# Performance work log

Hardware: AMD Instinct MI355X
Metric: run time of the kernel (lower is better)

Reference implementation:

```python
import jax, jax.numpy as jnp
import numpy as np

B, S, DIM = 2, 2048, 2048
NH, NKV = 16, 4
HD = DIM // NH
BASE, FACTOR = 10000.0, 1.0
WINDOW, STRIDE = 256, 64


def setup_inputs() -> dict:
    key = jax.random.key(0)
    ks = jax.random.split(key, 5)
    x = jax.random.normal(ks[0], (B, S, DIM), jnp.float32)
    Wq = jax.random.normal(ks[1], (DIM, DIM), jnp.float32) * 0.02
    Wkv = jax.random.normal(ks[2], (2 * NKV * HD, DIM), jnp.float32) * 0.02
    Wo = jax.random.normal(ks[3], (DIM, DIM), jnp.float32) * 0.02
    Wr = jax.random.normal(ks[4], (NH, DIM), jnp.float32) * 0.02
    br = jnp.zeros((NH,), jnp.float32)
    return {"x": x, "Wq": Wq, "Wkv": Wkv, "Wo": Wo, "Wr": Wr, "br": br}


def _rope_cos_sin(seqlen, start_pos):
    half = HD // 2
    inv_freq = 1.0 / (BASE ** (jnp.arange(0, half, dtype=jnp.float32) * 2.0 / HD))
    inv_freq = inv_freq / FACTOR  # YaRN position interpolation; FACTOR=1 -> vanilla RoPE
    mscale = float(0.1 * np.log(FACTOR) + 1.0) if FACTOR > 1.0 else 1.0
    t = jnp.arange(start_pos, start_pos + seqlen, dtype=jnp.float32)
    freqs = t[:, None] * inv_freq[None, :]  # [S, HD/2]
    return jnp.cos(freqs) * mscale, jnp.sin(freqs) * mscale


def _apply_rope(x, cos, sin):
    # x: [B, H, S, HD]; rotate-half convention
    x1, x2 = jnp.split(x, 2, axis=-1)
    return jnp.concatenate([x1 * cos - x2 * sin, x2 * cos + x1 * sin], axis=-1)


def reference(x, Wq, Wkv, Wo, Wr, br):
    scale = 1.0 / np.sqrt(HD)
    # projections
    q = (x @ Wq.T).reshape(B, S, NH, HD).transpose(0, 2, 1, 3)        # [B,NH,S,HD]
    kv = (x @ Wkv.T).reshape(B, S, 2, NKV, HD)
    k = kv[:, :, 0].transpose(0, 2, 1, 3)                              # [B,NKV,S,HD]
    v = kv[:, :, 1].transpose(0, 2, 1, 3)
    # RoPE (start_pos = 0)
    cos, sin = _rope_cos_sin(S, 0)
    cos, sin = cos[None, None], sin[None, None]
    q = _apply_rope(q, cos, sin)
    k = _apply_rope(k, cos, sin)
    # GQA expansion (repeat_interleave over head axis)
    rep = NH // NKV
    k = jnp.repeat(k, rep, axis=1)                                     # [B,NH,S,HD]
    v = jnp.repeat(v, rep, axis=1)
    # per-head sigmoid routing gate on q
    head_w = jax.nn.sigmoid(x @ Wr.T + br)                             # [B,S,NH]
    q = q * head_w.transpose(0, 2, 1)[..., None]
    # local windowed causal attention
    qi = jnp.arange(S)[:, None]
    ki = jnp.arange(S)[None, :]
    mask = (ki <= qi) & (ki >= qi - WINDOW)                            # [S,S]
    scores = jnp.einsum('bhqd,bhkd->bhqk', q, k) * scale
    scores = jnp.where(mask, scores, -1e30)
    attn_local = jnp.einsum('bhqk,bhkd->bhqd', jax.nn.softmax(scores, axis=-1), v)
    # strided global attention (non-causal over subsampled keys)
    g_idx = jnp.arange(0, S, STRIDE)
    kg, vg = k[:, :, g_idx], v[:, :, g_idx]                            # [B,NH,S/STRIDE,HD]
    gscores = jnp.einsum('bhqd,bhkd->bhqk', q, kg) * scale
    attn_global = jnp.einsum('bhqk,bhkd->bhqd', jax.nn.softmax(gscores, axis=-1), vg)
    out = 0.7 * attn_local + 0.3 * attn_global
    out = out.transpose(0, 2, 1, 3).reshape(B, S, DIM)
    return out @ Wo.T
```

## Files before the change

### kernel.cpp

```cpp
#include <hip/hip_runtime.h>
#include <stdint.h>

typedef unsigned short u16;
typedef uint32_t u32;
typedef __bf16 bf16x8 __attribute__((ext_vector_type(8)));
typedef u16    u16x8  __attribute__((ext_vector_type(8)));
typedef float  f32x4  __attribute__((ext_vector_type(4)));
typedef u32    u32x4v __attribute__((ext_vector_type(4)));

constexpr int Bc = 2, Sc = 2048, DIMc = 2048, NHc = 16, NKVc = 4, HDc = 128;
constexpr int Mc  = Bc * Sc;
constexpr int QKVN = 3072;
constexpr float SCALE = 0.08838834764831845f;

__device__ __forceinline__ u16 f2bf(float f) {
    uint32_t u = __builtin_bit_cast(uint32_t, f);
    u += 0x7FFFu + ((u >> 16) & 1u);
    return (u16)(u >> 16);
}
__device__ __forceinline__ u32 pk2bf(float a, float b) {
    return (u32)f2bf(a) | ((u32)f2bf(b) << 16);
}

__device__ __forceinline__ void async_cp16(const u16* gsrc, u16* ldst) {
    __builtin_amdgcn_global_load_lds(
        (__attribute__((address_space(1))) void*)(gsrc),
        (__attribute__((address_space(3))) void*)(ldst), 16, 0, 0);
}

constexpr int HWB = Mc;
constexpr int CQ1 = DIMc * DIMc / 4;
constexpr int CQ2 = 1024 * DIMc / 4;
constexpr int NWQ = (CQ1 + CQ2) / 256;
constexpr int NTB = Sc * 64 / 256;
__global__ __launch_bounds__(256) void cvt_hw(const float* __restrict__ x,
                                              const float* __restrict__ Wq,
                                              const float* __restrict__ Wkv,
                                              const float* __restrict__ Wr,
                                              const float* __restrict__ br,
                                              u16* __restrict__ xb,
                                              u16* __restrict__ Wqkvb,
                                              float* __restrict__ hw,
                                              float2* __restrict__ csT) {
    __shared__ __align__(16) float xs[2048];
    int bid = blockIdx.x;
    if (bid < HWB) {
        const int m = bid;
        const float4* xg = (const float4*)(x + (size_t)m * 2048);
        float4* xs4 = (float4*)xs;
        for (int i = threadIdx.x; i < 512; i += 256) xs4[i] = xg[i];
        __syncthreads();
        {
            ushort4* dst = (ushort4*)(xb + (size_t)m * 2048);
            for (int i = threadIdx.x; i < 512; i += 256) {
                float4 v = xs4[i];
                ushort4 o;
                o.x = f2bf(v.x); o.y = f2bf(v.y); o.z = f2bf(v.z); o.w = f2bf(v.w);
                dst[i] = o;
            }
        }
        const int wid = threadIdx.x >> 6, lane = threadIdx.x & 63;
#pragma unroll 1
        for (int h = wid; h < NHc; h += 4) {
            const float4* wr4 = (const float4*)(Wr + (size_t)h * 2048);
            float s = 0.f;
#pragma unroll
            for (int j = 0; j < 8; j++) {
                float4 xv = xs4[lane + j * 64];
                float4 wv = wr4[lane + j * 64];
                s += xv.x * wv.x + xv.y * wv.y + xv.z * wv.z + xv.w * wv.w;
            }
#pragma unroll
            for (int off = 32; off; off >>= 1) s += __shfl_xor(s, off, 64);
            if (lane == 0) hw[m * NHc + h] = 1.f / (1.f + __expf(-(s + br[h])));
        }
        return;
    }
    bid -= HWB;
    if (bid < NWQ) {
        int q = bid * 256 + threadIdx.x;
        const float* src; u16* dst; int qi;
        if (q < CQ1) { src = Wq;  dst = Wqkvb; qi = q; }
        else         { src = Wkv; dst = Wqkvb + (size_t)DIMc * DIMc; qi = q - CQ1; }
        float4 v = ((const float4*)src)[qi];
        ushort4 o;
        o.x = f2bf(v.x); o.y = f2bf(v.y); o.z = f2bf(v.z); o.w = f2bf(v.w);
        ((ushort4*)dst)[qi] = o;
        return;
    }
    bid -= NWQ;
    int idx = bid * 256 + threadIdx.x;
    int s = idx >> 6, d = idx & 63;
    float invf = powf(10000.0f, -(float)d * (1.0f / 64.0f));
    float ang = (float)s * invf;
    float2 cs;
    cs.x = cosf(ang);
    cs.y = sinf(ang);
    csT[idx] = cs;
}

__global__ __launch_bounds__(512, 2) void gemm_qkv(const u16* __restrict__ A,
                                                   const u16* __restrict__ Bw,
                                                   const float* __restrict__ hw,
                                                   const float2* __restrict__ csT,
                                                   const float* __restrict__ Wo,
                                                   u16* __restrict__ Wob,
                                                   u16* __restrict__ Qr,
                                                   u16* __restrict__ Kb,
                                                   u16* __restrict__ Vt,
                                                   u16* __restrict__ Vg) {
    const int bidL = blockIdx.x;
    if (bidL >= 192) {
        const float4* src = (const float4*)Wo;
        ushort4* dst = (ushort4*)Wob;
        int i0 = (bidL - 192) * 16384 + threadIdx.x;
#pragma unroll
        for (int k = 0; k < 32; k++) {
            float4 v = src[i0 + k * 512];
            ushort4 o;
            o.x = f2bf(v.x); o.y = f2bf(v.y); o.z = f2bf(v.z); o.w = f2bf(v.w);
            dst[i0 + k * 512] = o;
        }
        return;
    }
    __shared__ __align__(16) u16 SM[4][2][128 * 64];
    float* EpS = (float*)SM;
    const int Kd = DIMc;
    constexpr int NT = 32;
    const int tid  = threadIdx.x;
    const int lane = tid & 63;
    const int wid  = tid >> 6;
    const int m0 = (bidL / 12) * 256;
    const int n0 = (bidL % 12) * 256;
    const int wr = wid >> 2;
    const int wc = wid & 3;
    const int fr = lane & 15;
    const int fq = lane >> 4;
    const int f7 = fr & 7;

    const int s0 = tid, s1 = tid + 512;
    const int r0 = s0 >> 3, r1 = s1 >> 3;
    const int j0 = (s0 & 7) ^ (r0 & 7), j1 = (s1 & 7) ^ (r1 & 7);
    const u16* gA0 = A  + (size_t)(m0 + r0) * Kd + j0 * 8;
    const u16* gA1 = A  + (size_t)(m0 + r1) * Kd + j1 * 8;
    const u16* gB0 = Bw + (size_t)(n0 + r0) * Kd + j0 * 8;
    const u16* gB1 = Bw + (size_t)(n0 + r1) * Kd + j1 * 8;
    const size_t hK = (size_t)128 * Kd;

    auto stA = [&](int buf, int h, int t) {
        async_cp16(gA0 + h * hK + t * 64, &SM[buf][h][s0 * 8]);
        async_cp16(gA1 + h * hK + t * 64, &SM[buf][h][s1 * 8]);
    };
    auto stB = [&](int buf, int h, int t) {
        async_cp16(gB0 + h * hK + t * 64, &SM[2 + buf][h][s0 * 8]);
        async_cp16(gB1 + h * hK + t * 64, &SM[2 + buf][h][s1 * 8]);
    };

    f32x4 acc[8][4];
#pragma unroll
    for (int i = 0; i < 8; i++)
#pragma unroll
        for (int j = 0; j < 4; j++) {
            f32x4 z = {0.f, 0.f, 0.f, 0.f};
            acc[i][j] = z;
        }

    const int c0 = ((fq) ^ f7) * 8;
    const int c1 = ((4 + fq) ^ f7) * 8;
    bf16x8 afl[4][2], afh[4][2], bfl[2][2], bfh[2][2];

    auto rdA = [&](bf16x8 (&af)[4][2], int tb, int mh) {
        const u16* Ab = SM[tb][wr];
#pragma unroll
        for (int m2 = 0; m2 < 4; m2++) {
            int row = (mh * 4 + m2) * 16 + fr;
            af[m2][0] = __builtin_bit_cast(bf16x8, *(const u16x8*)(Ab + row * 64 + c0));
            af[m2][1] = __builtin_bit_cast(bf16x8, *(const u16x8*)(Ab + row * 64 + c1));
        }
    };
    auto rdB = [&](bf16x8 (&bf)[2][2], int tb, int nh) {
        const u16* Bb = SM[2 + tb][wc >> 1];
#pragma unroll
        for (int n2 = 0; n2 < 2; n2++) {
            int row = (wc & 1) * 64 + (nh * 2 + n2) * 16 + fr;
            bf[n2][0] = __builtin_bit_cast(bf16x8, *(const u16x8*)(Bb + row * 64 + c0));
            bf[n2][1] = __builtin_bit_cast(bf16x8, *(const u16x8*)(Bb + row * 64 + c1));
        }
    };
    auto mma = [&](bf16x8 (&af)[4][2], bf16x8 (&bf)[2][2], int mh, int nh) {
        __builtin_amdgcn_s_setprio(1);
#pragma unroll
        for (int m2 = 0; m2 < 4; m2++)
#pragma unroll
            for (int n2 = 0; n2 < 2; n2++) {
                acc[mh * 4 + m2][nh * 2 + n2] =
                    __builtin_amdgcn_mfma_f32_16x16x32_bf16(af[m2][0], bf[n2][0],
                                                            acc[mh * 4 + m2][nh * 2 + n2], 0, 0, 0);
                acc[mh * 4 + m2][nh * 2 + n2] =
                    __builtin_amdgcn_mfma_f32_16x16x32_bf16(af[m2][1], bf[n2][1],
                                                            acc[mh * 4 + m2][nh * 2 + n2], 0, 0, 0);
            }
        __builtin_amdgcn_s_setprio(0);
    };

#define LGK0 do { asm volatile("s_waitcnt lgkmcnt(0)" ::: "memory"); \
                  __builtin_amdgcn_sched_barrier(0); } while (0)
#define BAR  __builtin_amdgcn_s_barrier()

    stA(0, 0, 0); stA(0, 1, 0); stB(0, 0, 0); stB(0, 1, 0);
    stB(1, 0, 1); stB(1, 1, 1);
    asm volatile("s_waitcnt vmcnt(4)" ::: "memory");
    BAR;

#pragma unroll 1
    for (int i = 0; i < NT / 2; i++) {
        const int t0 = 2 * i, t1 = 2 * i + 1;
        rdA(afl, 0, 0); rdB(bfl, 0, 0);
        stA(1, 0, t1);
        BAR; LGK0; mma(afl, bfl, 0, 0); BAR;
        rdB(bfh, 0, 1);
        stA(1, 1, t1);
        BAR; LGK0; mma(afl, bfh, 0, 1); BAR;
        rdA(afh, 0, 1);
        if (t0 + 2 < NT) stB(0, 0, t0 + 2);
        BAR; LGK0; mma(afh, bfl, 1, 0); BAR;
        if (t0 + 2 < NT) {
            stB(0, 1, t0 + 2);
            asm volatile("s_waitcnt vmcnt(4)" ::: "memory");
        } else {
            asm volatile("s_waitcnt vmcnt(0)" ::: "memory");
        }
        BAR; __builtin_amdgcn_sched_barrier(0); mma(afh, bfh, 1, 1); BAR;
        rdA(afl, 1, 0); rdB(bfl, 1, 0);
        if (t0 + 2 < NT) stA(0, 0, t0 + 2);
        BAR; LGK0; mma(afl, bfl, 0, 0); BAR;
        rdB(bfh, 1, 1);
        if (t0 + 2 < NT) stA(0, 1, t0 + 2);
        BAR; LGK0; mma(afl, bfh, 0, 1); BAR;
        rdA(afh, 1, 1);
        if (t1 + 2 < NT) stB(1, 0, t1 + 2);
        BAR; LGK0; mma(afh, bfl, 1, 0); BAR;
        if (t1 + 2 < NT) {
            stB(1, 1, t1 + 2);
            asm volatile("s_waitcnt vmcnt(4)" ::: "memory");
        } else {
            asm volatile("s_waitcnt vmcnt(0)" ::: "memory");
        }
        BAR; __builtin_amdgcn_sched_barrier(0); mma(afh, bfh, 1, 1); BAR;
    }
#undef LGK0
#undef BAR

    const int tL = n0 >> 7;
    const int bb = m0 >> 11;
    const int sb_t = m0 & 2047;
#pragma unroll
    for (int p = 0; p < 4; p++) {
        __syncthreads();
        if (wr == (p >> 1)) {
#pragma unroll
            for (int m2 = 0; m2 < 4; m2++) {
#pragma unroll
                for (int nj = 0; nj < 4; nj++) {
                    int lr = m2 * 16 + fq * 4;
                    int col = wc * 64 + nj * 16 + fr;
#pragma unroll
                    for (int r = 0; r < 4; r++)
                        EpS[(lr + r) * 261 + col] = acc[(p & 1) * 4 + m2][nj][r];
                }
            }
        }
        __syncthreads();
        const int sbase = sb_t + p * 64;
        if (tL < 20) {
            const int d = tid & 63, rg = tid >> 6;
#pragma unroll 1
            for (int ch = 0; ch < 2; ch++) {
                const int t = tL + ch;
#pragma unroll
                for (int tt = 0; tt < 8; tt++) {
                    int lr = rg + 8 * tt;
                    int s = sbase + lr;
                    float v1 = EpS[lr * 261 + ch * 128 + d];
                    float v2 = EpS[lr * 261 + ch * 128 + 64 + d];
                    float2 cs = csT[(s << 6) + d];
                    float o1 = v1 * cs.x - v2 * cs.y;
                    float o2 = v2 * cs.x + v1 * cs.y;
                    if (t < 16) {
                        float w = hw[(size_t)((bb << 11) + s) * NHc + t] * SCALE;
                        size_t g = ((size_t)(bb * NHc + t) << 11) + s;
                        Qr[g * HDc + d]      = f2bf(o1 * w);
                        Qr[g * HDc + 64 + d] = f2bf(o2 * w);
                    } else {
                        size_t g = ((size_t)(bb * NKVc + (t - 16)) << 11) + s;
                        Kb[g * HDc + d]      = f2bf(o1);
                        Kb[g * HDc + 64 + d] = f2bf(o2);
                    }
                }
            }
        } else {
            const int sl = tid & 63, dg = tid >> 6;
            const int sg = sbase + sl;
#pragma unroll 1
            for (int ch = 0; ch < 2; ch++) {
                const int bhv = bb * NKVc + (tL + ch - 20);
                u16* Vbase = Vt + (size_t)bhv * HDc * Sc;
#pragma unroll
                for (int tt = 0; tt < 16; tt++) {
                    int d = dg + 8 * tt;
                    u16 bv = f2bf(EpS[sl * 261 + ch * 128 + d]);
                    Vbase[(size_t)d * Sc + sg] = bv;
                    if ((sg & 63) == 0)
                        Vg[(size_t)bhv * 4096 + d * 32 + (sg >> 6)] = bv;
                }
            }
        }
    }
}

__global__ __launch_bounds__(512, 2) void gemm_bt3(const u16* __restrict__ A,
                                                   const u16* __restrict__ Bw,
                                                   float* __restrict__ C,
                                                   int Mdim, int Ndim, int Kdim) {
    __shared__ __align__(16) u16 As[2][256 * 64];
    __shared__ __align__(16) u16 Bs[2][128 * 64];
    const int tid  = threadIdx.x;
    const int lane = tid & 63;
    const int wid  = tid >> 6;
    const int m0 = blockIdx.y * 256;
    const int n0 = blockIdx.x * 128;
    const int wm = (wid >> 1) * 64;
    const int wn = (wid & 1) * 64;
    const int fr = lane & 15;
    const int fq = lane >> 4;
    const int f7 = fr & 7;

    const u16* gA[4]; const u16* gB[2];
    int sOffA[4], sOffB[2];
#pragma unroll
    for (int q = 0; q < 4; q++) {
        int s = tid + q * 512;
        int row = s >> 3;
        int j = (s & 7) ^ (row & 7);
        gA[q] = A + (size_t)(m0 + row) * Kdim + j * 8;
        sOffA[q] = s * 8;
    }
#pragma unroll
    for (int q = 0; q < 2; q++) {
        int s = tid + q * 512;
        int row = s >> 3;
        int j = (s & 7) ^ (row & 7);
        gB[q] = Bw + (size_t)(n0 + row) * Kdim + j * 8;
        sOffB[q] = s * 8;
    }

    f32x4 acc[4][4];
#pragma unroll
    for (int i = 0; i < 4; i++)
#pragma unroll
        for (int j = 0; j < 4; j++) {
            f32x4 z = {0.f, 0.f, 0.f, 0.f};
            acc[i][j] = z;
        }

    const int NT = Kdim >> 6;
    const int c0 = ((fq) ^ f7) * 8;
    const int c1 = ((4 + fq) ^ f7) * 8;

#pragma unroll
    for (int q = 0; q < 4; q++) async_cp16(gA[q], &As[0][sOffA[q]]);
#pragma unroll
    for (int q = 0; q < 2; q++) async_cp16(gB[q], &Bs[0][sOffB[q]]);
#pragma unroll
    for (int q = 0; q < 4; q++) async_cp16(gA[q] + 64, &As[1][sOffA[q]]);
#pragma unroll
    for (int q = 0; q < 2; q++) async_cp16(gB[q] + 64, &Bs[1][sOffB[q]]);

    for (int t = 0; t < NT; t++) {
        const u16* At = As[t & 1];
        const u16* Bt = Bs[t & 1];

        if (t + 1 < NT) {
            asm volatile("s_waitcnt vmcnt(6)" ::: "memory");
        } else {
            asm volatile("s_waitcnt vmcnt(0)" ::: "memory");
        }
        __builtin_amdgcn_s_barrier();

        bf16x8 af0[4], bf0[4];
#pragma unroll
        for (int i = 0; i < 4; i++)
            af0[i] = __builtin_bit_cast(bf16x8, *(const u16x8*)(At + (wm + i * 16 + fr) * 64 + c0));
#pragma unroll
        for (int j = 0; j < 4; j++)
            bf0[j] = __builtin_bit_cast(bf16x8, *(const u16x8*)(Bt + (wn + j * 16 + fr) * 64 + c0));
        asm volatile("s_waitcnt lgkmcnt(0)" ::: "memory");
        __builtin_amdgcn_sched_barrier(0);
        __builtin_amdgcn_s_setprio(1);
#pragma unroll
        for (int i = 0; i < 2; i++)
#pragma unroll
            for (int j = 0; j < 4; j++)
                acc[i][j] = __builtin_amdgcn_mfma_f32_16x16x32_bf16(af0[i], bf0[j], acc[i][j], 0, 0, 0);
        __builtin_amdgcn_s_setprio(0);

        bf16x8 af1[4], bf1[4];
#pragma unroll
        for (int i = 0; i < 4; i++)
            af1[i] = __builtin_bit_cast(bf16x8, *(const u16x8*)(At + (wm + i * 16 + fr) * 64 + c1));
#pragma unroll
        for (int j = 0; j < 4; j++)
            bf1[j] = __builtin_bit_cast(bf16x8, *(const u16x8*)(Bt + (wn + j * 16 + fr) * 64 + c1));
        __builtin_amdgcn_s_setprio(1);
#pragma unroll
        for (int i = 2; i < 4; i++)
#pragma unroll
            for (int j = 0; j < 4; j++)
                acc[i][j] = __builtin_amdgcn_mfma_f32_16x16x32_bf16(af0[i], bf0[j], acc[i][j], 0, 0, 0);
        __builtin_amdgcn_s_setprio(0);
        asm volatile("s_waitcnt lgkmcnt(0)" ::: "memory");
        __builtin_amdgcn_sched_barrier(0);
        __builtin_amdgcn_s_barrier();

        if (t + 2 < NT) {
#pragma unroll
            for (int q = 0; q < 4; q++)
                async_cp16(gA[q] + (size_t)(t + 2) * 64, &As[t & 1][sOffA[q]]);
        }
        __builtin_amdgcn_s_setprio(1);
#pragma unroll
        for (int i = 0; i < 2; i++)
#pragma unroll
            for (int j = 0; j < 4; j++)
                acc[i][j] = __builtin_amdgcn_mfma_f32_16x16x32_bf16(af1[i], bf1[j], acc[i][j], 0, 0, 0);
        __builtin_amdgcn_s_setprio(0);

        if (t + 2 < NT) {
#pragma unroll
            for (int q = 0; q < 2; q++)
                async_cp16(gB[q] + (size_t)(t + 2) * 64, &Bs[t & 1][sOffB[q]]);
        }
        __builtin_amdgcn_s_setprio(1);
#pragma unroll
        for (int i = 2; i < 4; i++)
#pragma unroll
            for (int j = 0; j < 4; j++)
                acc[i][j] = __builtin_amdgcn_mfma_f32_16x16x32_bf16(af1[i], bf1[j], acc[i][j], 0, 0, 0);
        __builtin_amdgcn_s_setprio(0);
    }

#pragma unroll
    for (int i = 0; i < 4; i++)
#pragma unroll
        for (int j = 0; j < 4; j++) {
            int row = m0 + wm + i * 16 + fq * 4;
            int col = n0 + wn + j * 16 + fr;
#pragma unroll
            for (int r = 0; r < 4; r++)
                C[(size_t)(row + r) * Ndim + col] = acc[i][j][r];
        }
}

__device__ __forceinline__ float colreduce_max(f32x4 a, f32x4 b) {
    float m = fmaxf(fmaxf(fmaxf(a[0], a[1]), fmaxf(a[2], a[3])),
                    fmaxf(fmaxf(b[0], b[1]), fmaxf(b[2], b[3])));
    m = fmaxf(m, __shfl_xor(m, 16, 64));
    m = fmaxf(m, __shfl_xor(m, 32, 64));
    return m;
}

__device__ __forceinline__ bf16x8 build_pfrag(u32 pk0, u32 pk1, u32 pk2, u32 pk3, int lane) {
    const int c = lane & 15, Q = lane >> 4;
    const int sl0 = ((Q & 1) * 2) * 16 + c;
    const int sl1 = sl0 + 16;
    u32 a0 = (u32)__shfl((int)pk0, sl0, 64), b0 = (u32)__shfl((int)pk2, sl0, 64);
    u32 a1 = (u32)__shfl((int)pk1, sl0, 64), b1 = (u32)__shfl((int)pk3, sl0, 64);
    u32 a2 = (u32)__shfl((int)pk0, sl1, 64), b2 = (u32)__shfl((int)pk2, sl1, 64);
    u32 a3 = (u32)__shfl((int)pk1, sl1, 64), b3 = (u32)__shfl((int)pk3, sl1, 64);
    const bool hi = Q >= 2;
    u32x4v r = { hi ? b0 : a0, hi ? b1 : a1, hi ? b2 : a2, hi ? b3 : a3 };
    return __builtin_bit_cast(bf16x8, r);
}

__global__ __launch_bounds__(256) void attn3(const u16* __restrict__ Qr,
                                             const u16* __restrict__ Kb,
                                             const u16* __restrict__ Vt,
                                             const u16* __restrict__ Vg,
                                             u16* __restrict__ attnb) {
    __shared__ __align__(16) u16 Ksh[2 * 4096];
    __shared__ __align__(16) u16 Vsh[2 * 4096];
    const int tid  = threadIdx.x;
    const int lane = tid & 63, wid = tid >> 6;
    const int bid  = blockIdx.x;
    const int q64  = (31 - (bid >> 5)) << 6;
    const int bh   = bid & 31;
    const int h    = bh & 15;
    const int b    = bh >> 4;
    const int qw   = q64 + wid * 16;
    const int c = lane & 15, Q = lane >> 4;
    const int kvh = h >> 2;

    const u16* Qp = Qr + ((size_t)((b * NHc + h) * Sc + qw)) * HDc;
    const u16* Kh = Kb + (size_t)(b * NKVc + kvh) * Sc * HDc;
    const u16* Vh = Vt + (size_t)(b * NKVc + kvh) * HDc * Sc;
    const u16* Vgh = Vg + (size_t)(b * NKVc + kvh) * HDc * 32;

    const int kp0 = (q64 >= 256) ? (q64 - 256) : 0;
    const int nstages = (q64 + 64 - kp0) >> 5;

    auto stageLoad = [&](int bufi, int kp) {
        u16* Kd = Ksh + bufi * 4096;
        u16* Vd = Vsh + bufi * 4096;
#pragma unroll
        for (int qq = 0; qq < 2; qq++) {
            int s = tid + qq * 256;
            int kr = s >> 4;
            int jk = (s & 15) ^ (kr & 15);
            async_cp16(Kh + (size_t)(kp + kr) * HDc + jk * 8, Kd + s * 8);
            int dv = s >> 2;
            int jv = (s & 3) ^ ((dv >> 2) & 3);
            async_cp16(Vh + (size_t)dv * Sc + kp + jv * 8, Vd + s * 8);
        }
    };

    bf16x8 qf[4];
#pragma unroll
    for (int ch = 0; ch < 4; ch++)
        qf[ch] = __builtin_bit_cast(bf16x8, *(const u16x8*)(Qp + c * HDc + ch * 32 + Q * 8));

    stageLoad(0, kp0);

    f32x4 sg0 = {0.f,0.f,0.f,0.f}, sg1 = {0.f,0.f,0.f,0.f};
#pragma unroll
    for (int ch = 0; ch < 4; ch++) {
        bf16x8 k0 = __builtin_bit_cast(bf16x8, *(const u16x8*)(Kh + ((size_t)c << 6) * HDc + ch * 32 + Q * 8));
        bf16x8 k1 = __builtin_bit_cast(bf16x8, *(const u16x8*)(Kh + ((size_t)(c + 16) << 6) * HDc + ch * 32 + Q * 8));
        sg0 = __builtin_amdgcn_mfma_f32_16x16x32_bf16(k0, qf[ch], sg0, 0, 0, 0);
        sg1 = __builtin_amdgcn_mfma_f32_16x16x32_bf16(k1, qf[ch], sg1, 0, 0, 0);
    }
    float mg = colreduce_max(sg0, sg1);
    f32x4 pg0, pg1;
    float gsum = 0.f;
#pragma unroll
    for (int r = 0; r < 4; r++) {
        pg0[r] = __expf(sg0[r] - mg);
        pg1[r] = __expf(sg1[r] - mg);
        gsum += pg0[r] + pg1[r];
    }
    gsum += __shfl_xor(gsum, 16, 64);
    gsum += __shfl_xor(gsum, 32, 64);
    const float lG = gsum;
    bf16x8 pgf = build_pfrag(pk2bf(pg0[0], pg0[1]), pk2bf(pg0[2], pg0[3]),
                             pk2bf(pg1[0], pg1[1]), pk2bf(pg1[2], pg1[3]), lane);
    f32x4 OG[8];
#pragma unroll
    for (int dt = 0; dt < 8; dt++) {
        bf16x8 vf = __builtin_bit_cast(bf16x8, *(const u16x8*)(Vgh + (dt * 16 + c) * 32 + Q * 8));
        f32x4 z = {0.f, 0.f, 0.f, 0.f};
        OG[dt] = __builtin_amdgcn_mfma_f32_16x16x32_bf16(vf, pgf, z, 0, 0, 0);
    }

    f32x4 OL[8];
#pragma unroll
    for (int dt = 0; dt < 8; dt++) { f32x4 z = {0.f,0.f,0.f,0.f}; OL[dt] = z; }
    float mL = -1e30f, lL = 0.f;

    for (int ip = 0; ip < nstages; ip++) {
        const int kp = kp0 + ip * 32;
        __syncthreads();
        if (ip + 1 < nstages) stageLoad((ip + 1) & 1, kp + 32);
        const u16* Kd = Ksh + (ip & 1) * 4096;
        const u16* Vd = Vsh + (ip & 1) * 4096;

        if (kp > qw + 15 || kp + 31 < qw - 256) continue;

        f32x4 s0 = {0.f,0.f,0.f,0.f}, s1 = {0.f,0.f,0.f,0.f};
#pragma unroll
        for (int ch = 0; ch < 4; ch++) {
            int jj = ch * 4 + Q;
            bf16x8 k0 = __builtin_bit_cast(bf16x8, *(const u16x8*)(Kd + (c * 16 + (jj ^ c)) * 8));
            bf16x8 k1 = __builtin_bit_cast(bf16x8, *(const u16x8*)(Kd + ((16 + c) * 16 + (jj ^ c)) * 8));
            s0 = __builtin_amdgcn_mfma_f32_16x16x32_bf16(k0, qf[ch], s0, 0, 0, 0);
            s1 = __builtin_amdgcn_mfma_f32_16x16x32_bf16(k1, qf[ch], s1, 0, 0, 0);
        }
        if ((kp + 31 > qw) || (kp < qw - 241)) {
            const int q = qw + c;
#pragma unroll
            for (int r = 0; r < 4; r++) {
                int kk0 = kp + Q * 4 + r;
                int kk1 = kk0 + 16;
                if (kk0 > q || kk0 + 256 < q) s0[r] = -1e30f;
                if (kk1 > q || kk1 + 256 < q) s1[r] = -1e30f;
            }
        }
        float mx = colreduce_max(s0, s1);
        float mnew = fmaxf(mL, mx);
        float alpha = __expf(mL - mnew);
        f32x4 p0, p1;
        float sum = 0.f;
#pragma unroll
        for (int r = 0; r < 4; r++) {
            p0[r] = __expf(s0[r] - mnew);
            p1[r] = __expf(s1[r] - mnew);
            sum += p0[r] + p1[r];
        }
        sum += __shfl_xor(sum, 16, 64);
        sum += __shfl_xor(sum, 32, 64);
        lL = lL * alpha + sum;
        mL = mnew;
        bf16x8 pf = build_pfrag(pk2bf(p0[0], p0[1]), pk2bf(p0[2], p0[3]),
                                pk2bf(p1[0], p1[1]), pk2bf(p1[2], p1[3]), lane);
#pragma unroll
        for (int dt = 0; dt < 8; dt++) {
            int d = dt * 16 + c;
            bf16x8 vf = __builtin_bit_cast(bf16x8, *(const u16x8*)(Vd + (d * 4 + (Q ^ (c >> 2))) * 8));
            OL[dt] = OL[dt] * alpha;
            OL[dt] = __builtin_amdgcn_mfma_f32_16x16x32_bf16(vf, pf, OL[dt], 0, 0, 0);
        }
    }

    const float rL = 0.7f / lL, rG = 0.3f / lG;
    u16* orow = attnb + ((size_t)(b * Sc + qw + c)) * DIMc + h * HDc;
#pragma unroll
    for (int dt = 0; dt < 8; dt++) {
        ushort4 ov;
        ov.x = f2bf(OL[dt][0] * rL + OG[dt][0] * rG);
        ov.y = f2bf(OL[dt][1] * rL + OG[dt][1] * rG);
        ov.z = f2bf(OL[dt][2] * rL + OG[dt][2] * rG);
        ov.w = f2bf(OL[dt][3] * rL + OG[dt][3] * rG);
        *(ushort4*)(orow + dt * 16 + Q * 4) = ov;
    }
}

extern "C" void kernel_launch(void* const* d_in, const int* in_sizes, int n_in,
                              void* d_out, int out_size, void* d_ws, size_t ws_size,
                              hipStream_t stream) {
    const float* x   = (const float*)d_in[0];
    const float* Wq  = (const float*)d_in[1];
    const float* Wkv = (const float*)d_in[2];
    const float* Wo  = (const float*)d_in[3];
    const float* Wr  = (const float*)d_in[4];
    const float* br  = (const float*)d_in[5];
    float* out = (float*)d_out;

    char* p = (char*)d_ws;
    u16* xb    = (u16*)p;   p += (size_t)Mc * DIMc * 2;
    u16* Wqkvb = (u16*)p;   p += (size_t)QKVN * DIMc * 2;
    u16* Wob   = (u16*)p;   p += (size_t)DIMc * DIMc * 2;
    float* hw  = (float*)p; p += (size_t)Mc * NHc * 4;
    float2* csT = (float2*)p; p += (size_t)Sc * 64 * 8;
    u16* Qrb   = (u16*)p;   p += (size_t)Mc * DIMc * 2;
    u16* Kb16  = (u16*)p;   p += (size_t)Bc * NKVc * Sc * HDc * 2;
    u16* Vt16  = (u16*)p;   p += (size_t)Bc * NKVc * HDc * Sc * 2;
    u16* Vg16  = (u16*)p;   p += (size_t)Bc * NKVc * HDc * 32 * 2;
    u16* attnb = (u16*)p;   p += (size_t)Mc * DIMc * 2;

    cvt_hw<<<HWB + NWQ + NTB, 256, 0, stream>>>(x, Wq, Wkv, Wr, br, xb, Wqkvb, hw, csT);

    gemm_qkv<<<256, 512, 0, stream>>>(xb, Wqkvb, hw, csT, Wo, Wob, Qrb, Kb16, Vt16, Vg16);

    attn3<<<Bc * NHc * (Sc / 64), 256, 0, stream>>>(Qrb, Kb16, Vt16, Vg16, attnb);

    dim3 go(DIMc / 128, Mc / 256);
    gemm_bt3<<<go, 512, 0, stream>>>(attnb, Wob, out, Mc, DIMc, DIMc);
}
```

Measured before the change: 286.5 us.

## Restructure output-projection GEMM with 2x4 wave layout and fine-grained load/compute interleave

Replaces the output-projection GEMM kernel with a version that lays out 8 waves as 2x4 (each wave computes 128x32) instead of 4x2 (64x64). The K loop is split into eight phases per pair of K tiles, each staged with barriers, so A halves and B tiles are loaded asynchronously while each quarter of the MFMAs runs. The goal is to hide global-to-LDS latency better and smooth LDS read pressure. The cost is many more barriers per iteration and higher A-fragment register use. The scheme also only handles an even number of K tiles.

```diff
diff --git a/kernel.cpp b/kernel.cpp
--- a/kernel.cpp
+++ b/kernel.cpp
@@ -318,143 +318,134 @@
     }
 }
 
-__global__ __launch_bounds__(512, 2) void gemm_bt3(const u16* __restrict__ A,
+__global__ __launch_bounds__(512, 2) void gemm_bt4(const u16* __restrict__ A,
                                                    const u16* __restrict__ Bw,
                                                    float* __restrict__ C,
                                                    int Mdim, int Ndim, int Kdim) {
-    __shared__ __align__(16) u16 As[2][256 * 64];
-    __shared__ __align__(16) u16 Bs[2][128 * 64];
+    __shared__ __align__(16) u16 SA[2][2][128 * 64];
+    __shared__ __align__(16) u16 SB[2][128 * 64];
+    const int NT = Kdim >> 6;
     const int tid  = threadIdx.x;
     const int lane = tid & 63;
     const int wid  = tid >> 6;
     const int m0 = blockIdx.y * 256;
     const int n0 = blockIdx.x * 128;
-    const int wm = (wid >> 1) * 64;
-    const int wn = (wid & 1) * 64;
+    const int wr = wid >> 2;
+    const int wc = wid & 3;
     const int fr = lane & 15;
     const int fq = lane >> 4;
     const int f7 = fr & 7;
 
-    const u16* gA[4]; const u16* gB[2];
-    int sOffA[4], sOffB[2];
-#pragma unroll
-    for (int q = 0; q < 4; q++) {
-        int s = tid + q * 512;
-        int row = s >> 3;
-        int j = (s & 7) ^ (row & 7);
-        gA[q] = A + (size_t)(m0 + row) * Kdim + j * 8;
-        sOffA[q] = s * 8;
-    }
-#pragma unroll
-    for (int q = 0; q < 2; q++) {
-        int s = tid + q * 512;
-        int row = s >> 3;
-        int j = (s & 7) ^ (row & 7);
-        gB[q] = Bw + (size_t)(n0 + row) * Kdim + j * 8;
-        sOffB[q] = s * 8;
-    }
-
-    f32x4 acc[4][4];
-#pragma unroll
-    for (int i = 0; i < 4; i++)
-#pragma unroll
-        for (int j = 0; j < 4; j++) {
+    const int s0 = tid, s1 = tid + 512;
+    const int r0 = s0 >> 3, r1 = s1 >> 3;
+    const int j0 = (s0 & 7) ^ (r0 & 7), j1 = (s1 & 7) ^ (r1 & 7);
+    const u16* gA0 = A  + (size_t)(m0 + r0) * Kdim + j0 * 8;
+    const u16* gA1 = A  + (size_t)(m0 + r1) * Kdim + j1 * 8;
+    const u16* gB0 = Bw + (size_t)(n0 + r0) * Kdim + j0 * 8;
+    const u16* gB1 = Bw + (size_t)(n0 + r1) * Kdim + j1 * 8;
+    const size_t hK = (size_t)128 * Kdim;
+
+    auto stA = [&](int buf, int h, int t) {
+        async_cp16(gA0 + h * hK + t * 64, &SA[buf][h][s0 * 8]);
+        async_cp16(gA1 + h * hK + t * 64, &SA[buf][h][s1 * 8]);
+    };
+    auto stB = [&](int buf, int t) {
+        async_cp16(gB0 + t * 64, &SB[buf][s0 * 8]);
+        async_cp16(gB1 + t * 64, &SB[buf][s1 * 8]);
+    };
+
+    f32x4 acc[8][2];
+#pragma unroll
+    for (int i = 0; i < 8; i++)
+#pragma unroll
+        for (int j = 0; j < 2; j++) {
             f32x4 z = {0.f, 0.f, 0.f, 0.f};
             acc[i][j] = z;
         }
 
-    const int NT = Kdim >> 6;
     const int c0 = ((fq) ^ f7) * 8;
     const int c1 = ((4 + fq) ^ f7) * 8;
-
-#pragma unroll
-    for (int q = 0; q < 4; q++) async_cp16(gA[q], &As[0][sOffA[q]]);
-#pragma unroll
-    for (int q = 0; q < 2; q++) async_cp16(gB[q], &Bs[0][sOffB[q]]);
-#pragma unroll
-    for (int q = 0; q < 4; q++) async_cp16(gA[q] + 64, &As[1][sOffA[q]]);
-#pragma unroll
-    for (int q = 0; q < 2; q++) async_cp16(gB[q] + 64, &Bs[1][sOffB[q]]);
-
-    for (int t = 0; t < NT; t++) {
-        const u16* At = As[t & 1];
-        const u16* Bt = Bs[t & 1];
-
-        if (t + 1 < NT) {
-            asm volatile("s_waitcnt vmcnt(6)" ::: "memory");
+    bf16x8 afl[4][2], afh[4][2], bfl[2], bfh[2];
+
+    auto rdA = [&](bf16x8 (&af)[4][2], int tb, int mh) {
+        const u16* Ab = SA[tb][wr];
+#pragma unroll
+        for (int m2 = 0; m2 < 4; m2++) {
+            int row = (mh * 4 + m2) * 16 + fr;
+            af[m2][0] = __builtin_bit_cast(bf16x8, *(const u16x8*)(Ab + row * 64 + c0));
+            af[m2][1] = __builtin_bit_cast(bf16x8, *(const u16x8*)(Ab + row * 64 + c1));
+        }
+    };
+    auto rdB = [&](bf16x8 (&bf)[2], int tb, int nh) {
+        const u16* Bb = SB[tb];
+        int row = wc * 32 + nh * 16 + fr;
+        bf[0] = __builtin_bit_cast(bf16x8, *(const u16x8*)(Bb + row * 64 + c0));
+        bf[1] = __builtin_bit_cast(bf16x8, *(const u16x8*)(Bb + row * 64 + c1));
+    };
+    auto mma = [&](bf16x8 (&af)[4][2], bf16x8 (&bf)[2], int mh, int nh) {
+        __builtin_amdgcn_s_setprio(1);
+#pragma unroll
+        for (int m2 = 0; m2 < 4; m2++) {
+            acc[mh * 4 + m2][nh] = __builtin_amdgcn_mfma_f32_16x16x32_bf16(
+                af[m2][0], bf[0], acc[mh * 4 + m2][nh], 0, 0, 0);
+            acc[mh * 4 + m2][nh] = __builtin_amdgcn_mfma_f32_16x16x32_bf16(
+                af[m2][1], bf[1], acc[mh * 4 + m2][nh], 0, 0, 0);
+        }
+        __builtin_amdgcn_s_setprio(0);
+    };
+
+#define LGK0 do { asm volatile("s_waitcnt lgkmcnt(0)" ::: "memory"); \
+                  __builtin_amdgcn_sched_barrier(0); } while (0)
+#define BAR  __builtin_amdgcn_s_barrier()
+
+    stA(0, 0, 0); stA(0, 1, 0); stB(0, 0);
+    stB(1, 1);
+    asm volatile("s_waitcnt vmcnt(2)" ::: "memory");
+    BAR;
+
+#pragma unroll 1
+    for (int i = 0; i < NT / 2; i++) {
+        const int t0 = 2 * i, t1 = 2 * i + 1;
+        rdA(afl, 0, 0); rdB(bfl, 0, 0);
+        stA(1, 0, t1);
+        BAR; LGK0; mma(afl, bfl, 0, 0); BAR;
+        rdB(bfh, 0, 1);
+        stA(1, 1, t1);
+        BAR; LGK0; mma(afl, bfh, 0, 1); BAR;
+        rdA(afh, 0, 1);
+        if (t0 + 2 < NT) stB(0, t0 + 2);
+        BAR; LGK0; mma(afh, bfl, 1, 0); BAR;
+        if (t0 + 2 < NT) {
+            asm volatile("s_waitcnt vmcnt(2)" ::: "memory");
         } else {
             asm volatile("s_waitcnt vmcnt(0)" ::: "memory");
         }
-        __builtin_amdgcn_s_barrier();
-
-        bf16x8 af0[4], bf0[4];
-#pragma unroll
-        for (int i = 0; i < 4; i++)
-            af0[i] = __builtin_bit_cast(bf16x8, *(const u16x8*)(At + (wm + i * 16 + fr) * 64 + c0));
-#pragma unroll
-        for (int j = 0; j < 4; j++)
-            bf0[j] = __builtin_bit_cast(bf16x8, *(const u16x8*)(Bt + (wn + j * 16 + fr) * 64 + c0));
-        asm volatile("s_waitcnt lgkmcnt(0)" ::: "memory");
-        __builtin_amdgcn_sched_barrier(0);
-        __builtin_amdgcn_s_setprio(1);
-#pragma unroll
-        for (int i = 0; i < 2; i++)
-#pragma unroll
-            for (int j = 0; j < 4; j++)
-                acc[i][j] = __builtin_amdgcn_mfma_f32_16x16x32_bf16(af0[i], bf0[j], acc[i][j], 0, 0, 0);
-        __builtin_amdgcn_s_setprio(0);
-
-        bf16x8 af1[4], bf1[4];
-#pragma unroll
-        for (int i = 0; i < 4; i++)
-            af1[i] = __builtin_bit_cast(bf16x8, *(const u16x8*)(At + (wm + i * 16 + fr) * 64 + c1));
-#pragma unroll
-        for (int j = 0; j < 4; j++)
-            bf1[j] = __builtin_bit_cast(bf16x8, *(const u16x8*)(Bt + (wn + j * 16 + fr) * 64 + c1));
-        __builtin_amdgcn_s_setprio(1);
-#pragma unroll
-        for (int i = 2; i < 4; i++)
-#pragma unroll
-            for (int j = 0; j < 4; j++)
-                acc[i][j] = __builtin_amdgcn_mfma_f32_16x16x32_bf16(af0[i], bf0[j], acc[i][j], 0, 0, 0);
-        __builtin_amdgcn_s_setprio(0);
-        asm volatile("s_waitcnt lgkmcnt(0)" ::: "memory");
-        __builtin_amdgcn_sched_barrier(0);
-        __builtin_amdgcn_s_barrier();
-
-        if (t + 2 < NT) {
-#pragma unroll
-            for (int q = 0; q < 4; q++)
-                async_cp16(gA[q] + (size_t)(t + 2) * 64, &As[t & 1][sOffA[q]]);
-        }
-        __builtin_amdgcn_s_setprio(1);
-#pragma unroll
-        for (int i = 0; i < 2; i++)
-#pragma unroll
-            for (int j = 0; j < 4; j++)
-                acc[i][j] = __builtin_amdgcn_mfma_f32_16x16x32_bf16(af1[i], bf1[j], acc[i][j], 0, 0, 0);
-        __builtin_amdgcn_s_setprio(0);
-
-        if (t + 2 < NT) {
-#pragma unroll
-            for (int q = 0; q < 2; q++)
-                async_cp16(gB[q] + (size_t)(t + 2) * 64, &Bs[t & 1][sOffB[q]]);
-        }
-        __builtin_amdgcn_s_setprio(1);
-#pragma unroll
-        for (int i = 2; i < 4; i++)
-#pragma unroll
-            for (int j = 0; j < 4; j++)
-                acc[i][j] = __builtin_amdgcn_mfma_f32_16x16x32_bf16(af1[i], bf1[j], acc[i][j], 0, 0, 0);
-        __builtin_amdgcn_s_setprio(0);
-    }
-
-#pragma unroll
-    for (int i = 0; i < 4; i++)
-#pragma unroll
-        for (int j = 0; j < 4; j++) {
-            int row = m0 + wm + i * 16 + fq * 4;
-            int col = n0 + wn + j * 16 + fr;
+        BAR; __builtin_amdgcn_sched_barrier(0); mma(afh, bfh, 1, 1); BAR;
+        rdA(afl, 1, 0); rdB(bfl, 1, 0);
+        if (t0 + 2 < NT) stA(0, 0, t0 + 2);
+        BAR; LGK0; mma(afl, bfl, 0, 0); BAR;
+        rdB(bfh, 1, 1);
+        if (t0 + 2 < NT) stA(0, 1, t0 + 2);
+        BAR; LGK0; mma(afl, bfh, 0, 1); BAR;
+        rdA(afh, 1, 1);
+        if (t1 + 2 < NT) stB(1, t1 + 2);
+        BAR; LGK0; mma(afh, bfl, 1, 0); BAR;
+        if (t1 + 2 < NT) {
+            asm volatile("s_waitcnt vmcnt(2)" ::: "memory");
+        } else {
+            asm volatile("s_waitcnt vmcnt(0)" ::: "memory");
+        }
+        BAR; __builtin_amdgcn_sched_barrier(0); mma(afh, bfh, 1, 1); BAR;
+    }
+#undef LGK0
+#undef BAR
+
+#pragma unroll
+    for (int i = 0; i < 8; i++)
+#pragma unroll
+        for (int j = 0; j < 2; j++) {
+            int row = m0 + wr * 128 + i * 16 + fq * 4;
+            int col = n0 + wc * 32 + j * 16 + fr;
 #pragma unroll
             for (int r = 0; r < 4; r++)
                 C[(size_t)(row + r) * Ndim + col] = acc[i][j][r];
@@ -662,5 +653,5 @@
     attn3<<<Bc * NHc * (Sc / 64), 256, 0, stream>>>(Qrb, Kb16, Vt16, Vg16, attnb);
 
     dim3 go(DIMc / 128, Mc / 256);
-    gemm_bt3<<<go, 512, 0, stream>>>(attnb, Wob, out, Mc, DIMc, DIMc);
-}
+    gemm_bt4<<<go, 512, 0, stream>>>(attnb, Wob, out, Mc, DIMc, DIMc);
+}
```

Result: no change. 283.8 us (-0.9%).
